# Kernel optimization log

Hardware: AMD Instinct MI355X
Metric: run time of the kernel (lower is better)

The kernel has to match this reference:

```python
import jax, jax.numpy as jnp
import numpy as np

D_MODEL = 1024
NUM_HEADS = 16
D_HEAD = D_MODEL // NUM_HEADS  # 64
LAMBDA_INIT = 0.8
EPS = 1e-5


def setup_inputs() -> dict:
    key = jax.random.key(0)
    ks = jax.random.split(key, 10)
    B, N = 2, 2048
    # Xavier-uniform-ish scale for the projection weights
    def xav(k, shape):
        fan_in, fan_out = shape[0], shape[1]
        lim = np.sqrt(6.0 / (fan_in + fan_out))
        return jax.random.uniform(k, shape, jnp.float32, -lim, lim)
    return {
        "X": jax.random.normal(ks[0], (B, N, D_MODEL), jnp.float32),
        "Wq": xav(ks[1], (D_MODEL, 2 * D_MODEL)),
        "Wk": xav(ks[2], (D_MODEL, 2 * D_MODEL)),
        "Wv": xav(ks[3], (D_MODEL, 2 * D_MODEL)),
        "Wo": xav(ks[4], (2 * D_MODEL, D_MODEL)),
        "lambda_q1": jax.random.normal(ks[5], (NUM_HEADS, D_HEAD), jnp.float32),
        "lambda_k1": jax.random.normal(ks[6], (NUM_HEADS, D_HEAD), jnp.float32),
        "lambda_q2": jax.random.normal(ks[7], (NUM_HEADS, D_HEAD), jnp.float32),
        "lambda_k2": jax.random.normal(ks[8], (NUM_HEADS, D_HEAD), jnp.float32),
        "rms_scale": jnp.ones((2 * D_HEAD,), jnp.float32),
    }


def reference(X, Wq, Wk, Wv, Wo, lambda_q1, lambda_k1, lambda_q2, lambda_k2, rms_scale):
    B, N, _ = X.shape
    H, Dh = NUM_HEADS, D_HEAD
    # projections -> [B, H, N, 2*Dh]
    Q = (X @ Wq).reshape(B, N, H, 2 * Dh).transpose(0, 2, 1, 3)
    K = (X @ Wk).reshape(B, N, H, 2 * Dh).transpose(0, 2, 1, 3)
    V = (X @ Wv).reshape(B, N, H, 2 * Dh).transpose(0, 2, 1, 3)
    Q1, Q2 = Q[..., :Dh], Q[..., Dh:]
    K1, K2 = K[..., :Dh], K[..., Dh:]
    # learned lambda per head
    lam = (jnp.exp(jnp.sum(lambda_q1 * lambda_k1, -1))
           - jnp.exp(jnp.sum(lambda_q2 * lambda_k2, -1))
           + LAMBDA_INIT)  # [H]
    scaling = 1.0 / np.sqrt(Dh)
    causal = jnp.tril(jnp.ones((N, N), bool))  # [N, N]
    neg_inf = jnp.float32(-jnp.inf)
    A1 = jnp.einsum('bhqd,bhkd->bhqk', Q1, K1) * scaling
    A2 = jnp.einsum('bhqd,bhkd->bhqk', Q2, K2) * scaling
    A1 = jnp.where(causal, A1, neg_inf)
    A2 = jnp.where(causal, A2, neg_inf)
    attn = jax.nn.softmax(A1, axis=-1) - lam[None, :, None, None] * jax.nn.softmax(A2, axis=-1)
    O = jnp.einsum('bhqk,bhkd->bhqd', attn, V)  # [B, H, N, 2*Dh]
    # per-(batch,head,pos) RMSNorm over the 2*Dh channel dim
    rms = jnp.sqrt(jnp.mean(O * O, axis=-1, keepdims=True) + EPS)
    O = O / rms * rms_scale
    O = O * (1.0 - LAMBDA_INIT)
    O = O.transpose(0, 2, 1, 3).reshape(B, N, H * 2 * Dh)
    return O @ Wo
```

## Files before the change

kernel.cpp:

```cpp
#include <hip/hip_runtime.h>
#include <hip/hip_bf16.h>

#define DM   1024
#define NH   16
#define DH   64
#define NSEQ 2048
#define NBATCH 2
#define ROWS (NBATCH*NSEQ)
#define QKVN (2*DM)
#define STR3 (3*DM*2)

typedef __attribute__((ext_vector_type(8))) short short8;
typedef __attribute__((ext_vector_type(4))) float f32x4;
typedef __attribute__((ext_vector_type(4))) unsigned short u16x4;

__device__ __forceinline__ unsigned short f2bf(float x) {
  union { float f; unsigned u; } v; v.f = x;
  unsigned r = v.u + 0x7FFFu + ((v.u >> 16) & 1u);
  return (unsigned short)(r >> 16);
}

__device__ __forceinline__ float exp2a(float x) {
  float r; asm("v_exp_f32 %0, %1" : "=v"(r) : "v"(x)); return r;
}
__device__ __forceinline__ unsigned cvtpk(float lo, float hi) {
  unsigned d; asm("v_cvt_pk_bf16_f32 %0, %1, %2" : "=v"(d) : "v"(lo), "v"(hi)); return d;
}

__device__ __forceinline__ f32x4 mfma16(short8 a, short8 b, f32x4 c) {
  return __builtin_amdgcn_mfma_f32_16x16x32_bf16(a, b, c, 0, 0, 0);
}

#define GLL(src, dst) \
  __builtin_amdgcn_global_load_lds((const __attribute__((address_space(1))) void*)(src), \
                                   (__attribute__((address_space(3))) void*)(dst), 16, 0, 0)

__global__ void cast_f32_bf16(const float* __restrict__ in, unsigned short* __restrict__ out, int n4) {
  int i = blockIdx.x * blockDim.x + threadIdx.x;
  if (i >= n4) return;
  f32x4 v = *(const f32x4*)(in + (size_t)i * 4);
  u16x4 o;
  #pragma unroll
  for (int j = 0; j < 4; ++j) o[j] = f2bf(v[j]);
  *(u16x4*)(out + (size_t)i * 4) = o;
}

__global__ void transpose_cast_w(const float* __restrict__ in, unsigned short* __restrict__ out,
                                 int R, int C) {
  __shared__ float tile[32][33];
  const int bx = blockIdx.x, by = blockIdx.y;
  const int tx = threadIdx.x, ty = threadIdx.y;
  #pragma unroll
  for (int i = 0; i < 4; ++i)
    tile[ty + i*8][tx] = in[(size_t)(by*32 + ty + i*8) * C + bx*32 + tx];
  __syncthreads();
  #pragma unroll
  for (int i = 0; i < 4; ++i)
    out[(size_t)(bx*32 + ty + i*8) * R + by*32 + tx] = f2bf(tile[tx][ty + i*8]);
}

__global__ void lam_kernel(const float* __restrict__ lq1, const float* __restrict__ lk1,
                           const float* __restrict__ lq2, const float* __restrict__ lk2,
                           float* __restrict__ lam) {
  int h = threadIdx.x >> 6, lane = threadIdx.x & 63;
  float p1 = lq1[h*64 + lane] * lk1[h*64 + lane];
  float p2 = lq2[h*64 + lane] * lk2[h*64 + lane];
  #pragma unroll
  for (int mk = 32; mk >= 1; mk >>= 1) {
    p1 += __shfl_xor(p1, mk);
    p2 += __shfl_xor(p2, mk);
  }
  if (lane == 0) lam[h] = expf(p1) - expf(p2) + 0.8f;
}

template <typename OT, bool FUSEV>
__global__ __launch_bounds__(256) void gemm_bt(const unsigned short* __restrict__ A,
                                               const unsigned short* __restrict__ Bt,
                                               OT* __restrict__ C,
                                               unsigned short* __restrict__ VtOut,
                                               int M, int N, int K, int ldc) {
  __shared__ __align__(16) unsigned short As[128*32];
  __shared__ __align__(16) unsigned short Bs[128*32];
  const int tid = threadIdx.x;
  const int w = tid >> 6, lane = tid & 63;
  const int l15 = lane & 15, lg = lane >> 4;
  const int wr = w >> 1, wc = w & 1;

  const unsigned gx = gridDim.x;
  unsigned bid = blockIdx.y * gx + blockIdx.x;
  const unsigned cpx = (gx * gridDim.y) >> 3;
  bid = (bid & 7u) * cpx + (bid >> 3);
  const int m0 = (int)(bid / gx) * 128, n0 = (int)(bid % gx) * 128;

  f32x4 acc[4][4];
  #pragma unroll
  for (int i = 0; i < 4; ++i)
    #pragma unroll
    for (int j = 0; j < 4; ++j) acc[i][j] = f32x4{0.f, 0.f, 0.f, 0.f};

  for (int kt = 0; kt < K; kt += 32) {
    #pragma unroll
    for (int j = 0; j < 2; ++j) {
      int cbase = (j*4 + w) * 64;
      int c = cbase + lane;
      const unsigned short* ga = A + (size_t)(m0 + (c >> 2)) * K + kt + (c & 3) * 8;
      GLL(ga, As + cbase*8);
      const unsigned short* gb = Bt + (size_t)(n0 + (c >> 2)) * K + kt + (c & 3) * 8;
      GLL(gb, Bs + cbase*8);
    }
    __syncthreads();
    short8 af[4], bfr[4];
    #pragma unroll
    for (int m = 0; m < 4; ++m)
      af[m] = *(const short8*)(As + (wr*64 + m*16 + l15) * 32 + lg*8);
    #pragma unroll
    for (int n = 0; n < 4; ++n)
      bfr[n] = *(const short8*)(Bs + (wc*64 + n*16 + l15) * 32 + lg*8);
    #pragma unroll
    for (int m = 0; m < 4; ++m)
      #pragma unroll
      for (int n = 0; n < 4; ++n)
        acc[m][n] = mfma16(af[m], bfr[n], acc[m][n]);
    __syncthreads();
  }

  if (FUSEV && n0 >= 4096) {
    #pragma unroll
    for (int m = 0; m < 4; ++m) {
      const int row = m0 + wr*64 + m*16 + lg*4;
      const int b = row >> 11, nn = row & 2047;
      #pragma unroll
      for (int n = 0; n < 4; ++n) {
        const int vcol = (n0 - 4096) + wc*64 + n*16 + l15;
        const int h = vcol >> 7, dd = vcol & 127;
        u16x4 o;
        #pragma unroll
        for (int r = 0; r < 4; ++r) o[r] = f2bf(acc[m][n][r]);
        *(u16x4*)(VtOut + ((size_t)((b*NH + h)*128 + dd)) * NSEQ + nn) = o;
      }
    }
  } else {
    #pragma unroll
    for (int m = 0; m < 4; ++m)
      #pragma unroll
      for (int n = 0; n < 4; ++n)
        #pragma unroll
        for (int r = 0; r < 4; ++r) {
          int row = m0 + wr*64 + m*16 + lg*4 + r;
          int col = n0 + wc*64 + n*16 + l15;
          if constexpr (sizeof(OT) == 2)
            C[(size_t)row * ldc + col] = f2bf(acc[m][n][r]);
          else
            C[(size_t)row * ldc + col] = acc[m][n][r];
        }
  }
}

__global__ __launch_bounds__(256) void diff_attn(const unsigned short* __restrict__ QK,
                                                 const unsigned short* __restrict__ Vt,
                                                 const float* __restrict__ lam_arr,
                                                 const float* __restrict__ rms_scale,
                                                 unsigned short* __restrict__ O) {
  __shared__ __align__(16) unsigned short Ks[2][64*128];
  __shared__ __align__(16) unsigned short Vs[2][128*64];
  __shared__ __align__(16) unsigned short Plds[4][2][16*64];

  const unsigned bid = blockIdx.x;
  const int xcd = (int)(bid & 7u), idx = (int)(bid >> 3);
  const int bh = xcd * 4 + (idx >> 4);
  const int jj = idx & 15;

  const int b = bh >> 4, h = bh & 15;
  const int w = threadIdx.x >> 6, lane = threadIdx.x & 63;
  const int l15 = lane & 15, lg = lane >> 4;
  const float lam = lam_arr[h];

  const unsigned short* Qb  = QK + (size_t)(b * NSEQ) * 4096 + h * 128;
  const unsigned short* Kb  = QK + (size_t)(b * NSEQ) * 4096 + 2048 + h * 128;
  const unsigned short* Vtb = Vt + (size_t)bh * 128 * NSEQ;

  auto stage = [&](int bufi, int key0) {
    #pragma unroll
    for (int j = 0; j < 4; ++j) {
      const int t = j*4 + w;
      {
        const int row = t*4 + (lane >> 4);
        const int ck  = lane & 15;
        const int cks = (ck & 8) | ((ck ^ row) & 7);
        GLL(Kb + (size_t)(key0 + row) * 4096 + cks*8, &Ks[bufi][t*512]);
      }
      {
        const int row = t*8 + (lane >> 3);
        const int ck  = lane & 7;
        const int cks = (ck ^ row) & 7;
        GLL(Vtb + (size_t)row * NSEQ + key0 + cks*8, &Vs[bufi][t*512]);
      }
    }
  };

  char* pb0 = (char*)&Plds[w][0][0];
  char* pb1 = (char*)&Plds[w][1][0];
  const unsigned swz = (unsigned)((l15 & 7) << 4);
  const float qsc = 0.125f * 1.44269504088896340736f;

  for (int pass = 0; pass < 2; ++pass) {
    const int qt = pass ? jj : 31 - jj;
    const int q0 = qt * 64 + w * 16;

    short8 a1[2], a2[2];
    #pragma unroll
    for (int kc = 0; kc < 2; ++kc) {
      const unsigned short* qp = Qb + (size_t)(q0 + l15) * 4096 + kc*32 + lg*8;
      short8 r1 = *(const short8*)qp;
      short8 r2 = *(const short8*)(qp + 64);
      #pragma unroll
      for (int j = 0; j < 8; j += 2) {
        union { unsigned u; float f; } x0, x1, y0, y1;
        x0.u = ((unsigned)(unsigned short)r1[j]) << 16;
        x1.u = ((unsigned)(unsigned short)r1[j+1]) << 16;
        y0.u = ((unsigned)(unsigned short)r2[j]) << 16;
        y1.u = ((unsigned)(unsigned short)r2[j+1]) << 16;
        unsigned d1 = cvtpk(x0.f * qsc, x1.f * qsc);
        unsigned d2 = cvtpk(y0.f * qsc, y1.f * qsc);
        a1[kc][j]   = (short)(unsigned short)(d1 & 0xffffu);
        a1[kc][j+1] = (short)(unsigned short)(d1 >> 16);
        a2[kc][j]   = (short)(unsigned short)(d2 & 0xffffu);
        a2[kc][j+1] = (short)(unsigned short)(d2 >> 16);
      }
    }

    f32x4 o1[8], o2[8];
    #pragma unroll
    for (int i = 0; i < 8; ++i) { o1[i] = f32x4{0,0,0,0}; o2[i] = f32x4{0,0,0,0}; }
    float m1 = -3e38f, l1 = 0.f, m2 = -3e38f, l2 = 0.f;

    stage(0, 0);
    __syncthreads();
    int buf = 0;

    for (int kb = 0; kb <= qt; ++kb) {
      const int key0 = kb * 64;
      if (kb < qt) stage(buf ^ 1, key0 + 64);

      f32x4 st1[4], st2[4];
      #pragma unroll
      for (int nb = 0; nb < 4; ++nb) { st1[nb] = f32x4{0,0,0,0}; st2[nb] = f32x4{0,0,0,0}; }
      __builtin_amdgcn_s_setprio(1);
      #pragma unroll
      for (int nb = 0; nb < 4; ++nb) {
        const int row = nb*16 + l15;
        #pragma unroll
        for (int kc = 0; kc < 2; ++kc) {
          const unsigned short* kp = &Ks[buf][row*128 + (((kc*4 + lg) ^ row) & 7) * 8];
          short8 bk1 = *(const short8*)kp;
          short8 bk2 = *(const short8*)(kp + 64);
          st1[nb] = mfma16(bk1, a1[kc], st1[nb]);
          st2[nb] = mfma16(bk2, a2[kc], st2[nb]);
        }
      }
      __builtin_amdgcn_s_setprio(0);

      if (kb == qt) {
        #pragma unroll
        for (int nb = 0; nb < 4; ++nb)
          #pragma unroll
          for (int r = 0; r < 4; ++r)
            if (key0 + nb*16 + lg*4 + r > q0 + l15) { st1[nb][r] = -3e38f; st2[nb][r] = -3e38f; }
      }

      float tm1 = -3e38f, tm2 = -3e38f;
      #pragma unroll
      for (int nb = 0; nb < 4; ++nb)
        #pragma unroll
        for (int r = 0; r < 4; ++r) {
          tm1 = fmaxf(tm1, st1[nb][r]); tm2 = fmaxf(tm2, st2[nb][r]);
        }
      tm1 = fmaxf(tm1, __shfl_xor(tm1, 16));
      tm1 = fmaxf(tm1, __shfl_xor(tm1, 32));
      tm2 = fmaxf(tm2, __shfl_xor(tm2, 16));
      tm2 = fmaxf(tm2, __shfl_xor(tm2, 32));

      if (__any(tm1 > m1 + 8.f)) {
        const float nm = fmaxf(m1, tm1);
        const float e = exp2a(m1 - nm);
        m1 = nm; l1 *= e;
        float er[4];
        #pragma unroll
        for (int r = 0; r < 4; ++r) er[r] = __shfl(e, lg*4 + r);
        #pragma unroll
        for (int i = 0; i < 8; ++i)
          #pragma unroll
          for (int r = 0; r < 4; ++r) o1[i][r] *= er[r];
      }
      if (__any(tm2 > m2 + 8.f)) {
        const float nm = fmaxf(m2, tm2);
        const float e = exp2a(m2 - nm);
        m2 = nm; l2 *= e;
        float er[4];
        #pragma unroll
        for (int r = 0; r < 4; ++r) er[r] = __shfl(e, lg*4 + r);
        #pragma unroll
        for (int i = 0; i < 8; ++i)
          #pragma unroll
          for (int r = 0; r < 4; ++r) o2[i][r] *= er[r];
      }

      float ts1 = 0.f, ts2 = 0.f;
      #pragma unroll
      for (int nb = 0; nb < 4; ++nb)
        #pragma unroll
        for (int r = 0; r < 4; ++r) {
          st1[nb][r] = exp2a(st1[nb][r] - m1); ts1 += st1[nb][r];
          st2[nb][r] = exp2a(st2[nb][r] - m2); ts2 += st2[nb][r];
        }
      ts1 += __shfl_xor(ts1, 16); ts1 += __shfl_xor(ts1, 32); l1 += ts1;
      ts2 += __shfl_xor(ts2, 16); ts2 += __shfl_xor(ts2, 32); l2 += ts2;

      #pragma unroll
      for (int nb = 0; nb < 4; ++nb) {
        const unsigned off = (unsigned)(l15*128 + nb*32 + lg*8) ^ swz;
        *(uint2*)(pb0 + off) = make_uint2(cvtpk(st1[nb][0], st1[nb][1]),
                                          cvtpk(st1[nb][2], st1[nb][3]));
        *(uint2*)(pb1 + off) = make_uint2(cvtpk(st2[nb][0], st2[nb][1]),
                                          cvtpk(st2[nb][2], st2[nb][3]));
      }
      asm volatile("s_waitcnt lgkmcnt(0)" ::: "memory");
      __builtin_amdgcn_sched_barrier(0);
      short8 pa1[2], pa2[2];
      #pragma unroll
      for (int kc = 0; kc < 2; ++kc) {
        const unsigned off = (unsigned)(l15*128 + kc*64 + lg*16) ^ swz;
        pa1[kc] = *(const short8*)(pb0 + off);
        pa2[kc] = *(const short8*)(pb1 + off);
      }
      __builtin_amdgcn_sched_barrier(0);

      __builtin_amdgcn_s_setprio(1);
      #pragma unroll
      for (int i = 0; i < 8; ++i) {
        const int row = i*16 + l15;
        #pragma unroll
        for (int kc = 0; kc < 2; ++kc) {
          const short8 bv = *(const short8*)(&Vs[buf][row*64 + (((kc*4 + lg) ^ row) & 7) * 8]);
          o1[i] = mfma16(pa1[kc], bv, o1[i]);
          o2[i] = mfma16(pa2[kc], bv, o2[i]);
        }
      }
      __builtin_amdgcn_s_setprio(0);

      __syncthreads();
      buf ^= 1;
    }

    float i1r[4], i2r[4];
    {
      const float inv1 = 1.f / l1, inv2 = 1.f / l2;
      #pragma unroll
      for (int r = 0; r < 4; ++r) {
        i1r[r] = __shfl(inv1, lg*4 + r);
        i2r[r] = __shfl(inv2, lg*4 + r);
      }
    }
    float ov[8][4];
    float ssq[4] = {0.f, 0.f, 0.f, 0.f};
    #pragma unroll
    for (int i = 0; i < 8; ++i)
      #pragma unroll
      for (int r = 0; r < 4; ++r) {
        float v = o1[i][r] * i1r[r] - lam * (o2[i][r] * i2r[r]);
        ov[i][r] = v;
        ssq[r] += v * v;
      }
    #pragma unroll
    for (int r = 0; r < 4; ++r)
      #pragma unroll
      for (int mk = 1; mk < 16; mk <<= 1) ssq[r] += __shfl_xor(ssq[r], mk);
    float rr[4];
    #pragma unroll
    for (int r = 0; r < 4; ++r) rr[r] = rsqrtf(ssq[r] * (1.f/128.f) + 1e-5f) * 0.2f;
    #pragma unroll
    for (int i = 0; i < 8; ++i) {
      const float sc = rms_scale[i*16 + l15];
      #pragma unroll
      for (int r = 0; r < 4; ++r) {
        const int q = q0 + lg*4 + r;
        O[(size_t)(b*NSEQ + q) * QKVN + h*128 + i*16 + l15] = f2bf(ov[i][r] * rr[r] * sc);
      }
    }
  }
}

extern "C" void kernel_launch(void* const* d_in, const int* in_sizes, int n_in,
                              void* d_out, int out_size, void* d_ws, size_t ws_size,
                              hipStream_t stream) {
  (void)in_sizes; (void)n_in; (void)out_size; (void)ws_size;
  const float* X   = (const float*)d_in[0];
  const float* Wq  = (const float*)d_in[1];
  const float* Wk  = (const float*)d_in[2];
  const float* Wv  = (const float*)d_in[3];
  const float* Wo  = (const float*)d_in[4];
  const float* lq1 = (const float*)d_in[5];
  const float* lk1 = (const float*)d_in[6];
  const float* lq2 = (const float*)d_in[7];
  const float* lk2 = (const float*)d_in[8];
  const float* rs  = (const float*)d_in[9];
  float* out = (float*)d_out;

  char* ws = (char*)d_ws;
  const size_t MB = 1ull << 20;
  unsigned short* Xb  = (unsigned short*)(ws);
  unsigned short* Wt  = (unsigned short*)(ws + 8*MB);
  unsigned short* Wot = (unsigned short*)(ws + 20*MB);
  unsigned short* QK  = (unsigned short*)(ws + 24*MB);
  unsigned short* Ob  = (unsigned short*)(ws + 56*MB);
  unsigned short* Vt  = (unsigned short*)(ws + 72*MB);
  float*          lamp = (float*)(ws + 88*MB);

  cast_f32_bf16<<<(ROWS*DM/4 + 255)/256, 256, 0, stream>>>(X, Xb, ROWS*DM/4);
  transpose_cast_w<<<dim3(QKVN/32, DM/32), dim3(32,8), 0, stream>>>(Wq, Wt,             DM, QKVN);
  transpose_cast_w<<<dim3(QKVN/32, DM/32), dim3(32,8), 0, stream>>>(Wk, Wt + 2048*1024, DM, QKVN);
  transpose_cast_w<<<dim3(QKVN/32, DM/32), dim3(32,8), 0, stream>>>(Wv, Wt + 4096*1024, DM, QKVN);
  transpose_cast_w<<<dim3(DM/32, QKVN/32), dim3(32,8), 0, stream>>>(Wo, Wot, QKVN, DM);
  lam_kernel<<<1, 1024, 0, stream>>>(lq1, lk1, lq2, lk2, lamp);

  gemm_bt<unsigned short, true><<<dim3(STR3/128, ROWS/128), 256, 0, stream>>>(
      Xb, Wt, QK, Vt, ROWS, STR3, DM, 4096);

  diff_attn<<<dim3(512), 256, 0, stream>>>(QK, Vt, lamp, rs, Ob);

  gemm_bt<float, false><<<dim3(DM/128, ROWS/128), 256, 0, stream>>>(
      Ob, Wot, out, nullptr, ROWS, DM, QKVN, DM);
}
```

Before: 247.8 us.

## Split attention into one q-tile per block, load V directly from global

Each block now handles a single query tile instead of a paired long and short tile, and the grid doubles to 1024 blocks, which are ordered longest-first. V is no longer staged in LDS; it is read straight from global memory into registers for the PV MFMAs. This halves shared-memory use, and launch bounds request 3 blocks per CU to raise occupancy. The risk is extra global-load latency on V and worse load balance without the pairing trick.

```diff
diff --git a/kernel.cpp b/kernel.cpp
--- a/kernel.cpp
+++ b/kernel.cpp
@@ -156,45 +156,37 @@
   }
 }
 
-__global__ __launch_bounds__(256) void diff_attn(const unsigned short* __restrict__ QK,
-                                                 const unsigned short* __restrict__ Vt,
-                                                 const float* __restrict__ lam_arr,
-                                                 const float* __restrict__ rms_scale,
-                                                 unsigned short* __restrict__ O) {
+__global__ __launch_bounds__(256, 3) void diff_attn(const unsigned short* __restrict__ QK,
+                                                    const unsigned short* __restrict__ Vt,
+                                                    const float* __restrict__ lam_arr,
+                                                    const float* __restrict__ rms_scale,
+                                                    unsigned short* __restrict__ O) {
   __shared__ __align__(16) unsigned short Ks[2][64*128];
-  __shared__ __align__(16) unsigned short Vs[2][128*64];
   __shared__ __align__(16) unsigned short Plds[4][2][16*64];
 
   const unsigned bid = blockIdx.x;
   const int xcd = (int)(bid & 7u), idx = (int)(bid >> 3);
-  const int bh = xcd * 4 + (idx >> 4);
-  const int jj = idx & 15;
+  const int bh  = xcd * 4 + (idx & 3);
+  const int yy  = 31 - (idx >> 2);
 
   const int b = bh >> 4, h = bh & 15;
   const int w = threadIdx.x >> 6, lane = threadIdx.x & 63;
   const int l15 = lane & 15, lg = lane >> 4;
+  const int q0 = yy * 64 + w * 16;
   const float lam = lam_arr[h];
 
   const unsigned short* Qb  = QK + (size_t)(b * NSEQ) * 4096 + h * 128;
   const unsigned short* Kb  = QK + (size_t)(b * NSEQ) * 4096 + 2048 + h * 128;
   const unsigned short* Vtb = Vt + (size_t)bh * 128 * NSEQ;
 
-  auto stage = [&](int bufi, int key0) {
+  auto stageK = [&](int bufi, int key0) {
     #pragma unroll
     for (int j = 0; j < 4; ++j) {
       const int t = j*4 + w;
-      {
-        const int row = t*4 + (lane >> 4);
-        const int ck  = lane & 15;
-        const int cks = (ck & 8) | ((ck ^ row) & 7);
-        GLL(Kb + (size_t)(key0 + row) * 4096 + cks*8, &Ks[bufi][t*512]);
-      }
-      {
-        const int row = t*8 + (lane >> 3);
-        const int ck  = lane & 7;
-        const int cks = (ck ^ row) & 7;
-        GLL(Vtb + (size_t)row * NSEQ + key0 + cks*8, &Vs[bufi][t*512]);
-      }
+      const int row = t*4 + (lane >> 4);
+      const int ck  = lane & 15;
+      const int cks = (ck & 8) | ((ck ^ row) & 7);
+      GLL(Kb + (size_t)(key0 + row) * 4096 + cks*8, &Ks[bufi][t*512]);
     }
   };
 
@@ -202,190 +194,202 @@
   char* pb1 = (char*)&Plds[w][1][0];
   const unsigned swz = (unsigned)((l15 & 7) << 4);
   const float qsc = 0.125f * 1.44269504088896340736f;
-
-  for (int pass = 0; pass < 2; ++pass) {
-    const int qt = pass ? jj : 31 - jj;
-    const int q0 = qt * 64 + w * 16;
-
-    short8 a1[2], a2[2];
-    #pragma unroll
-    for (int kc = 0; kc < 2; ++kc) {
-      const unsigned short* qp = Qb + (size_t)(q0 + l15) * 4096 + kc*32 + lg*8;
-      short8 r1 = *(const short8*)qp;
-      short8 r2 = *(const short8*)(qp + 64);
-      #pragma unroll
-      for (int j = 0; j < 8; j += 2) {
-        union { unsigned u; float f; } x0, x1, y0, y1;
-        x0.u = ((unsigned)(unsigned short)r1[j]) << 16;
-        x1.u = ((unsigned)(unsigned short)r1[j+1]) << 16;
-        y0.u = ((unsigned)(unsigned short)r2[j]) << 16;
-        y1.u = ((unsigned)(unsigned short)r2[j+1]) << 16;
-        unsigned d1 = cvtpk(x0.f * qsc, x1.f * qsc);
-        unsigned d2 = cvtpk(y0.f * qsc, y1.f * qsc);
-        a1[kc][j]   = (short)(unsigned short)(d1 & 0xffffu);
-        a1[kc][j+1] = (short)(unsigned short)(d1 >> 16);
-        a2[kc][j]   = (short)(unsigned short)(d2 & 0xffffu);
-        a2[kc][j+1] = (short)(unsigned short)(d2 >> 16);
-      }
-    }
-
-    f32x4 o1[8], o2[8];
-    #pragma unroll
-    for (int i = 0; i < 8; ++i) { o1[i] = f32x4{0,0,0,0}; o2[i] = f32x4{0,0,0,0}; }
-    float m1 = -3e38f, l1 = 0.f, m2 = -3e38f, l2 = 0.f;
-
-    stage(0, 0);
-    __syncthreads();
-    int buf = 0;
-
-    for (int kb = 0; kb <= qt; ++kb) {
-      const int key0 = kb * 64;
-      if (kb < qt) stage(buf ^ 1, key0 + 64);
-
-      f32x4 st1[4], st2[4];
-      #pragma unroll
-      for (int nb = 0; nb < 4; ++nb) { st1[nb] = f32x4{0,0,0,0}; st2[nb] = f32x4{0,0,0,0}; }
-      __builtin_amdgcn_s_setprio(1);
-      #pragma unroll
-      for (int nb = 0; nb < 4; ++nb) {
-        const int row = nb*16 + l15;
-        #pragma unroll
-        for (int kc = 0; kc < 2; ++kc) {
-          const unsigned short* kp = &Ks[buf][row*128 + (((kc*4 + lg) ^ row) & 7) * 8];
-          short8 bk1 = *(const short8*)kp;
-          short8 bk2 = *(const short8*)(kp + 64);
-          st1[nb] = mfma16(bk1, a1[kc], st1[nb]);
-          st2[nb] = mfma16(bk2, a2[kc], st2[nb]);
-        }
-      }
-      __builtin_amdgcn_s_setprio(0);
-
-      if (kb == qt) {
-        #pragma unroll
-        for (int nb = 0; nb < 4; ++nb)
-          #pragma unroll
-          for (int r = 0; r < 4; ++r)
-            if (key0 + nb*16 + lg*4 + r > q0 + l15) { st1[nb][r] = -3e38f; st2[nb][r] = -3e38f; }
-      }
-
-      float tm1 = -3e38f, tm2 = -3e38f;
+  const int kx0 = ((lg ^ l15) & 7) * 8;
+  const int kx1 = (((4 + lg) ^ l15) & 7) * 8;
+
+  short8 a1[2], a2[2];
+  #pragma unroll
+  for (int kc = 0; kc < 2; ++kc) {
+    const unsigned short* qp = Qb + (size_t)(q0 + l15) * 4096 + kc*32 + lg*8;
+    short8 r1 = *(const short8*)qp;
+    short8 r2 = *(const short8*)(qp + 64);
+    #pragma unroll
+    for (int j = 0; j < 8; j += 2) {
+      union { unsigned u; float f; } x0, x1, y0, y1;
+      x0.u = ((unsigned)(unsigned short)r1[j]) << 16;
+      x1.u = ((unsigned)(unsigned short)r1[j+1]) << 16;
+      y0.u = ((unsigned)(unsigned short)r2[j]) << 16;
+      y1.u = ((unsigned)(unsigned short)r2[j+1]) << 16;
+      unsigned d1 = cvtpk(x0.f * qsc, x1.f * qsc);
+      unsigned d2 = cvtpk(y0.f * qsc, y1.f * qsc);
+      a1[kc][j]   = (short)(unsigned short)(d1 & 0xffffu);
+      a1[kc][j+1] = (short)(unsigned short)(d1 >> 16);
+      a2[kc][j]   = (short)(unsigned short)(d2 & 0xffffu);
+      a2[kc][j+1] = (short)(unsigned short)(d2 >> 16);
+    }
+  }
+
+  f32x4 o1[8], o2[8];
+  #pragma unroll
+  for (int i = 0; i < 8; ++i) { o1[i] = f32x4{0,0,0,0}; o2[i] = f32x4{0,0,0,0}; }
+  float m1 = -3e38f, l1 = 0.f, m2 = -3e38f, l2 = 0.f;
+
+  stageK(0, 0);
+  __syncthreads();
+  int buf = 0;
+
+  for (int kb = 0; kb <= yy; ++kb) {
+    const int key0 = kb * 64;
+    if (kb < yy) stageK(buf ^ 1, key0 + 64);
+
+    f32x4 st1[4], st2[4];
+    #pragma unroll
+    for (int nb = 0; nb < 4; ++nb) { st1[nb] = f32x4{0,0,0,0}; st2[nb] = f32x4{0,0,0,0}; }
+    __builtin_amdgcn_s_setprio(1);
+    #pragma unroll
+    for (int nb = 0; nb < 4; ++nb) {
+      const unsigned short* krow = &Ks[buf][nb*2048 + l15*128];
+      short8 k10 = *(const short8*)(krow + kx0);
+      short8 k11 = *(const short8*)(krow + kx1);
+      short8 k20 = *(const short8*)(krow + kx0 + 64);
+      short8 k21 = *(const short8*)(krow + kx1 + 64);
+      st1[nb] = mfma16(k10, a1[0], st1[nb]);
+      st1[nb] = mfma16(k11, a1[1], st1[nb]);
+      st2[nb] = mfma16(k20, a2[0], st2[nb]);
+      st2[nb] = mfma16(k21, a2[1], st2[nb]);
+    }
+    __builtin_amdgcn_s_setprio(0);
+
+    short8 bva[4][2];
+    #pragma unroll
+    for (int i = 0; i < 4; ++i) {
+      const unsigned short* vp = Vtb + (size_t)(i*16 + l15) * NSEQ + key0 + lg*8;
+      bva[i][0] = *(const short8*)vp;
+      bva[i][1] = *(const short8*)(vp + 32);
+    }
+
+    if (kb == yy) {
       #pragma unroll
       for (int nb = 0; nb < 4; ++nb)
         #pragma unroll
-        for (int r = 0; r < 4; ++r) {
-          tm1 = fmaxf(tm1, st1[nb][r]); tm2 = fmaxf(tm2, st2[nb][r]);
-        }
-      tm1 = fmaxf(tm1, __shfl_xor(tm1, 16));
-      tm1 = fmaxf(tm1, __shfl_xor(tm1, 32));
-      tm2 = fmaxf(tm2, __shfl_xor(tm2, 16));
-      tm2 = fmaxf(tm2, __shfl_xor(tm2, 32));
-
-      if (__any(tm1 > m1 + 8.f)) {
-        const float nm = fmaxf(m1, tm1);
-        const float e = exp2a(m1 - nm);
-        m1 = nm; l1 *= e;
-        float er[4];
+        for (int r = 0; r < 4; ++r)
+          if (key0 + nb*16 + lg*4 + r > q0 + l15) { st1[nb][r] = -3e38f; st2[nb][r] = -3e38f; }
+    }
+
+    float tm1 = -3e38f, tm2 = -3e38f;
+    #pragma unroll
+    for (int nb = 0; nb < 4; ++nb)
+      #pragma unroll
+      for (int r = 0; r < 4; ++r) {
+        tm1 = fmaxf(tm1, st1[nb][r]); tm2 = fmaxf(tm2, st2[nb][r]);
+      }
+    tm1 = fmaxf(tm1, __shfl_xor(tm1, 16));
+    tm1 = fmaxf(tm1, __shfl_xor(tm1, 32));
+    tm2 = fmaxf(tm2, __shfl_xor(tm2, 16));
+    tm2 = fmaxf(tm2, __shfl_xor(tm2, 32));
+
+    if (__any(tm1 > m1 + 8.f)) {
+      const float nm = fmaxf(m1, tm1);
+      const float e = exp2a(m1 - nm);
+      m1 = nm; l1 *= e;
+      float er[4];
+      #pragma unroll
+      for (int r = 0; r < 4; ++r) er[r] = __shfl(e, lg*4 + r);
+      #pragma unroll
+      for (int i = 0; i < 8; ++i)
         #pragma unroll
-        for (int r = 0; r < 4; ++r) er[r] = __shfl(e, lg*4 + r);
+        for (int r = 0; r < 4; ++r) o1[i][r] *= er[r];
+    }
+    if (__any(tm2 > m2 + 8.f)) {
+      const float nm = fmaxf(m2, tm2);
+      const float e = exp2a(m2 - nm);
+      m2 = nm; l2 *= e;
+      float er[4];
+      #pragma unroll
+      for (int r = 0; r < 4; ++r) er[r] = __shfl(e, lg*4 + r);
+      #pragma unroll
+      for (int i = 0; i < 8; ++i)
         #pragma unroll
-        for (int i = 0; i < 8; ++i)
-          #pragma unroll
-          for (int r = 0; r < 4; ++r) o1[i][r] *= er[r];
+        for (int r = 0; r < 4; ++r) o2[i][r] *= er[r];
+    }
+
+    float ts1 = 0.f, ts2 = 0.f;
+    #pragma unroll
+    for (int nb = 0; nb < 4; ++nb)
+      #pragma unroll
+      for (int r = 0; r < 4; ++r) {
+        st1[nb][r] = exp2a(st1[nb][r] - m1); ts1 += st1[nb][r];
+        st2[nb][r] = exp2a(st2[nb][r] - m2); ts2 += st2[nb][r];
       }
-      if (__any(tm2 > m2 + 8.f)) {
-        const float nm = fmaxf(m2, tm2);
-        const float e = exp2a(m2 - nm);
-        m2 = nm; l2 *= e;
-        float er[4];
-        #pragma unroll
-        for (int r = 0; r < 4; ++r) er[r] = __shfl(e, lg*4 + r);
-        #pragma unroll
-        for (int i = 0; i < 8; ++i)
-          #pragma unroll
-          for (int r = 0; r < 4; ++r) o2[i][r] *= er[r];
-      }
-
-      float ts1 = 0.f, ts2 = 0.f;
-      #pragma unroll
-      for (int nb = 0; nb < 4; ++nb)
-        #pragma unroll
-        for (int r = 0; r < 4; ++r) {
-          st1[nb][r] = exp2a(st1[nb][r] - m1); ts1 += st1[nb][r];
-          st2[nb][r] = exp2a(st2[nb][r] - m2); ts2 += st2[nb][r];
-        }
-      ts1 += __shfl_xor(ts1, 16); ts1 += __shfl_xor(ts1, 32); l1 += ts1;
-      ts2 += __shfl_xor(ts2, 16); ts2 += __shfl_xor(ts2, 32); l2 += ts2;
-
-      #pragma unroll
-      for (int nb = 0; nb < 4; ++nb) {
-        const unsigned off = (unsigned)(l15*128 + nb*32 + lg*8) ^ swz;
-        *(uint2*)(pb0 + off) = make_uint2(cvtpk(st1[nb][0], st1[nb][1]),
-                                          cvtpk(st1[nb][2], st1[nb][3]));
-        *(uint2*)(pb1 + off) = make_uint2(cvtpk(st2[nb][0], st2[nb][1]),
-                                          cvtpk(st2[nb][2], st2[nb][3]));
-      }
-      asm volatile("s_waitcnt lgkmcnt(0)" ::: "memory");
-      __builtin_amdgcn_sched_barrier(0);
-      short8 pa1[2], pa2[2];
-      #pragma unroll
-      for (int kc = 0; kc < 2; ++kc) {
-        const unsigned off = (unsigned)(l15*128 + kc*64 + lg*16) ^ swz;
-        pa1[kc] = *(const short8*)(pb0 + off);
-        pa2[kc] = *(const short8*)(pb1 + off);
-      }
-      __builtin_amdgcn_sched_barrier(0);
-
-      __builtin_amdgcn_s_setprio(1);
-      #pragma unroll
-      for (int i = 0; i < 8; ++i) {
-        const int row = i*16 + l15;
-        #pragma unroll
-        for (int kc = 0; kc < 2; ++kc) {
-          const short8 bv = *(const short8*)(&Vs[buf][row*64 + (((kc*4 + lg) ^ row) & 7) * 8]);
-          o1[i] = mfma16(pa1[kc], bv, o1[i]);
-          o2[i] = mfma16(pa2[kc], bv, o2[i]);
-        }
-      }
-      __builtin_amdgcn_s_setprio(0);
-
-      __syncthreads();
-      buf ^= 1;
-    }
-
-    float i1r[4], i2r[4];
-    {
-      const float inv1 = 1.f / l1, inv2 = 1.f / l2;
-      #pragma unroll
-      for (int r = 0; r < 4; ++r) {
-        i1r[r] = __shfl(inv1, lg*4 + r);
-        i2r[r] = __shfl(inv2, lg*4 + r);
-      }
-    }
-    float ov[8][4];
-    float ssq[4] = {0.f, 0.f, 0.f, 0.f};
-    #pragma unroll
-    for (int i = 0; i < 8; ++i)
-      #pragma unroll
-      for (int r = 0; r < 4; ++r) {
-        float v = o1[i][r] * i1r[r] - lam * (o2[i][r] * i2r[r]);
-        ov[i][r] = v;
-        ssq[r] += v * v;
-      }
-    #pragma unroll
-    for (int r = 0; r < 4; ++r)
-      #pragma unroll
-      for (int mk = 1; mk < 16; mk <<= 1) ssq[r] += __shfl_xor(ssq[r], mk);
-    float rr[4];
-    #pragma unroll
-    for (int r = 0; r < 4; ++r) rr[r] = rsqrtf(ssq[r] * (1.f/128.f) + 1e-5f) * 0.2f;
-    #pragma unroll
-    for (int i = 0; i < 8; ++i) {
-      const float sc = rms_scale[i*16 + l15];
-      #pragma unroll
-      for (int r = 0; r < 4; ++r) {
-        const int q = q0 + lg*4 + r;
-        O[(size_t)(b*NSEQ + q) * QKVN + h*128 + i*16 + l15] = f2bf(ov[i][r] * rr[r] * sc);
-      }
+    ts1 += __shfl_xor(ts1, 16); ts1 += __shfl_xor(ts1, 32); l1 += ts1;
+    ts2 += __shfl_xor(ts2, 16); ts2 += __shfl_xor(ts2, 32); l2 += ts2;
+
+    #pragma unroll
+    for (int nb = 0; nb < 4; ++nb) {
+      const unsigned off = (unsigned)(l15*128 + nb*32 + lg*8) ^ swz;
+      *(uint2*)(pb0 + off) = make_uint2(cvtpk(st1[nb][0], st1[nb][1]),
+                                        cvtpk(st1[nb][2], st1[nb][3]));
+      *(uint2*)(pb1 + off) = make_uint2(cvtpk(st2[nb][0], st2[nb][1]),
+                                        cvtpk(st2[nb][2], st2[nb][3]));
+    }
+    asm volatile("s_waitcnt lgkmcnt(0)" ::: "memory");
+    __builtin_amdgcn_sched_barrier(0);
+    short8 pa1[2], pa2[2];
+    #pragma unroll
+    for (int kc = 0; kc < 2; ++kc) {
+      const unsigned off = (unsigned)(l15*128 + kc*64 + lg*16) ^ swz;
+      pa1[kc] = *(const short8*)(pb0 + off);
+      pa2[kc] = *(const short8*)(pb1 + off);
+    }
+    __builtin_amdgcn_sched_barrier(0);
+
+    __builtin_amdgcn_s_setprio(1);
+    #pragma unroll
+    for (int i = 0; i < 4; ++i) {
+      o1[i] = mfma16(pa1[0], bva[i][0], o1[i]);
+      o2[i] = mfma16(pa2[0], bva[i][0], o2[i]);
+      o1[i] = mfma16(pa1[1], bva[i][1], o1[i]);
+      o2[i] = mfma16(pa2[1], bva[i][1], o2[i]);
+    }
+    #pragma unroll
+    for (int i = 4; i < 8; ++i) {
+      const unsigned short* vp = Vtb + (size_t)(i*16 + l15) * NSEQ + key0 + lg*8;
+      const short8 b0 = *(const short8*)vp;
+      const short8 b1 = *(const short8*)(vp + 32);
+      o1[i] = mfma16(pa1[0], b0, o1[i]);
+      o2[i] = mfma16(pa2[0], b0, o2[i]);
+      o1[i] = mfma16(pa1[1], b1, o1[i]);
+      o2[i] = mfma16(pa2[1], b1, o2[i]);
+    }
+    __builtin_amdgcn_s_setprio(0);
+
+    __syncthreads();
+    buf ^= 1;
+  }
+
+  float i1r[4], i2r[4];
+  {
+    const float inv1 = 1.f / l1, inv2 = 1.f / l2;
+    #pragma unroll
+    for (int r = 0; r < 4; ++r) {
+      i1r[r] = __shfl(inv1, lg*4 + r);
+      i2r[r] = __shfl(inv2, lg*4 + r);
+    }
+  }
+  float ov[8][4];
+  float ssq[4] = {0.f, 0.f, 0.f, 0.f};
+  #pragma unroll
+  for (int i = 0; i < 8; ++i)
+    #pragma unroll
+    for (int r = 0; r < 4; ++r) {
+      float v = o1[i][r] * i1r[r] - lam * (o2[i][r] * i2r[r]);
+      ov[i][r] = v;
+      ssq[r] += v * v;
+    }
+  #pragma unroll
+  for (int r = 0; r < 4; ++r)
+    #pragma unroll
+    for (int mk = 1; mk < 16; mk <<= 1) ssq[r] += __shfl_xor(ssq[r], mk);
+  float rr[4];
+  #pragma unroll
+  for (int r = 0; r < 4; ++r) rr[r] = rsqrtf(ssq[r] * (1.f/128.f) + 1e-5f) * 0.2f;
+  #pragma unroll
+  for (int i = 0; i < 8; ++i) {
+    const float sc = rms_scale[i*16 + l15];
+    #pragma unroll
+    for (int r = 0; r < 4; ++r) {
+      const int q = q0 + lg*4 + r;
+      O[(size_t)(b*NSEQ + q) * QKVN + h*128 + i*16 + l15] = f2bf(ov[i][r] * rr[r] * sc);
     }
   }
 }
@@ -426,7 +430,7 @@
   gemm_bt<unsigned short, true><<<dim3(STR3/128, ROWS/128), 256, 0, stream>>>(
       Xb, Wt, QK, Vt, ROWS, STR3, DM, 4096);
 
-  diff_attn<<<dim3(512), 256, 0, stream>>>(QK, Vt, lamp, rs, Ob);
+  diff_attn<<<dim3(1024), 256, 0, stream>>>(QK, Vt, lamp, rs, Ob);
 
   gemm_bt<float, false><<<dim3(DM/128, ROWS/128), 256, 0, stream>>>(
       Ob, Wot, out, nullptr, ROWS, DM, QKVN, DM);
```

Result: slower. 368.3 us (+48.7%).
